# Performance work log

Hardware: AMD Instinct MI355X
Metric: run time of the kernel (lower is better)

The kernel has to match this reference:

```python
import jax, jax.numpy as jnp
import numpy as np

B, T, C = 2, 2048, 2048
NH, NKV = 16, 4
HD = C // NH  # 128


def setup_inputs() -> dict:
    key = jax.random.key(0)
    ks = jax.random.split(key, 5)
    w = lambda k, shape: jax.random.normal(k, shape, jnp.float32) * 0.02
    return {
        "x": jax.random.normal(ks[0], (B, T, C), jnp.float32),
        "Wq": w(ks[1], (C, C)),
        "Wk": w(ks[2], (C, NKV * HD)),
        "Wv": w(ks[3], (C, NKV * HD)),
        "Wproj": w(ks[4], (C, C)),
    }


def _rope(x):
    # x: [B, H, T, D]; rotate-half RoPE with base 10000
    D = x.shape[-1]
    t = x.shape[-2]
    inv_freq = 1.0 / (10000.0 ** (jnp.arange(0, D, 2, dtype=jnp.float32) / D))
    freqs = jnp.arange(t, dtype=jnp.float32)[:, None] * inv_freq[None, :]  # [T, D/2]
    emb = jnp.concatenate([freqs, freqs], axis=-1)  # [T, D]
    cos, sin = jnp.cos(emb), jnp.sin(emb)
    x1, x2 = x[..., : D // 2], x[..., D // 2 :]
    rotated = jnp.concatenate([-x2, x1], axis=-1)
    return x * cos + rotated * sin


def reference(x, Wq, Wk, Wv, Wproj):
    b, t, c = x.shape
    q = (x @ Wq).reshape(b, t, NH, HD).transpose(0, 2, 1, 3)    # [B,NH,T,HD]
    k = (x @ Wk).reshape(b, t, NKV, HD).transpose(0, 2, 1, 3)   # [B,NKV,T,HD]
    v = (x @ Wv).reshape(b, t, NKV, HD).transpose(0, 2, 1, 3)
    q = _rope(q)
    k = _rope(k)
    rep = NH // NKV
    k = jnp.repeat(k, rep, axis=1)  # [B,NH,T,HD]
    v = jnp.repeat(v, rep, axis=1)
    scale = 1.0 / jnp.sqrt(jnp.float32(HD))
    scores = jnp.einsum("bhqd,bhkd->bhqk", q, k) * scale        # [B,NH,T,T]
    causal = jnp.tril(jnp.ones((t, t), dtype=bool))
    scores = jnp.where(causal, scores, jnp.finfo(scores.dtype).min)
    attn = jax.nn.softmax(scores, axis=-1)
    y = jnp.einsum("bhqk,bhkd->bhqd", attn, v)                  # [B,NH,T,HD]
    y = y.transpose(0, 2, 1, 3).reshape(b, t, c)
    return y @ Wproj
```

## Files before the change

kernel.cpp:

```cpp
#include <hip/hip_runtime.h>

#define B_ 2
#define T_ 2048
#define C_ 2048
#define NH_ 16
#define NKV_ 4
#define HD_ 128
#define M_ 4096
#define NQKV_ 3072

typedef __bf16 bf16x8 __attribute__((ext_vector_type(8)));
typedef float f32x4 __attribute__((ext_vector_type(4)));
typedef float f32x16 __attribute__((ext_vector_type(16)));

__device__ __forceinline__ unsigned short f2bf(float f) {
  union { float f; unsigned u; } c{f};
  unsigned u = c.u + 0x7FFFu + ((c.u >> 16) & 1u);
  return (unsigned short)(u >> 16);
}
__device__ __forceinline__ float bf2f(unsigned short h) {
  union { unsigned u; float f; } c{(unsigned)h << 16};
  return c.f;
}

#define GLOAD_LDS16(g, l)                                        \
  __builtin_amdgcn_global_load_lds(                              \
      (const __attribute__((address_space(1))) void*)(g),        \
      (__attribute__((address_space(3))) void*)(l), 16, 0, 0)

__global__ void rope_table_kernel(float2* __restrict__ rt) {
  int t = blockIdx.x, i = threadIdx.x;
  float inv = powf(10000.f, -(float)(2 * i) / 128.f);
  float s, c;
  sincosf((float)t * inv, &s, &c);
  rt[t * 64 + i] = make_float2(c, s);
}

__global__ void convx_kernel(const float* __restrict__ x, unsigned short* __restrict__ xb, int n4) {
  int i = blockIdx.x * blockDim.x + threadIdx.x;
  if (i >= n4) return;
  float4 v = reinterpret_cast<const float4*>(x)[i];
  union { ushort4 u; unsigned short s[4]; } o;
  o.s[0] = f2bf(v.x); o.s[1] = f2bf(v.y); o.s[2] = f2bf(v.z); o.s[3] = f2bf(v.w);
  reinterpret_cast<ushort4*>(xb)[i] = o.u;
}

__global__ void transpose_conv_kernel(const float* __restrict__ W, unsigned short* __restrict__ Wt,
                                      int K, int N) {
  __shared__ float tile[32][33];
  int bx = blockIdx.x * 32;
  int by = blockIdx.y * 32;
  int tx = threadIdx.x & 31, ty = threadIdx.x >> 5;
#pragma unroll
  for (int r = 0; r < 32; r += 8)
    tile[ty + r][tx] = W[(size_t)(by + ty + r) * N + bx + tx];
  __syncthreads();
#pragma unroll
  for (int r = 0; r < 32; r += 8)
    Wt[(size_t)(bx + ty + r) * K + by + tx] = f2bf(tile[tx][ty + r]);
}

__global__ void rope_kernel(unsigned short* __restrict__ qkv, const float2* __restrict__ rt) {
  int g = blockIdx.x * blockDim.x + threadIdx.x;
  if (g >= M_ * 160) return;
  int m = g / 160, u = g - m * 160;
  int t = m & (T_ - 1);
  int io, col0;
  if (u < 128) { io = (u & 7) * 8; col0 = (u >> 3) * HD_ + io; }
  else         { int uu = u - 128; io = (uu & 7) * 8; col0 = C_ + (uu >> 3) * HD_ + io; }
  unsigned short* p = qkv + (size_t)m * NQKV_ + col0;
  union V8 { uint4 v; unsigned short s[8]; };
  V8 a, b, oa, ob;
  a.v = *reinterpret_cast<const uint4*>(p);
  b.v = *reinterpret_cast<const uint4*>(p + 64);
#pragma unroll
  for (int j = 0; j < 8; ++j) {
    float2 cs = rt[t * 64 + io + j];
    float x1 = bf2f(a.s[j]), x2 = bf2f(b.s[j]);
    oa.s[j] = f2bf(x1 * cs.x - x2 * cs.y);
    ob.s[j] = f2bf(x2 * cs.x + x1 * cs.y);
  }
  *reinterpret_cast<uint4*>(p) = oa.v;
  *reinterpret_cast<uint4*>(p + 64) = ob.v;
}

__global__ void transpose_v_kernel(const unsigned short* __restrict__ qkv,
                                   unsigned short* __restrict__ vt) {
  __shared__ unsigned short tile[32][33];
  int bh = blockIdx.z;
  int b = bh >> 2, kvh = bh & 3;
  int t0 = blockIdx.x * 32, d0 = blockIdx.y * 32;
  int tx = threadIdx.x & 31, ty = threadIdx.x >> 5;
#pragma unroll
  for (int r = 0; r < 32; r += 8)
    tile[ty + r][tx] = qkv[(size_t)(b * T_ + t0 + ty + r) * NQKV_ + 2560 + kvh * HD_ + d0 + tx];
  __syncthreads();
#pragma unroll
  for (int r = 0; r < 32; r += 8)
    vt[(size_t)(bh * HD_ + d0 + ty + r) * T_ + t0 + tx] = tile[tx][ty + r];
}

template <typename OUT>
__global__ __launch_bounds__(256) void gemm_bf16(const unsigned short* __restrict__ A,
                                                 const unsigned short* __restrict__ Bt,
                                                 OUT* __restrict__ Cm,
                                                 int M, int N, int K) {
  constexpr int BK = 32;
  __shared__ __align__(16) unsigned short Al[2][128 * BK];
  __shared__ __align__(16) unsigned short Bl[2][128 * BK];
  int tid = threadIdx.x, w = tid >> 6, lane = tid & 63;
  int l15 = lane & 15, l4 = lane >> 4;
  int wr = w >> 1, wc = w & 1;
  size_t arow0 = (size_t)blockIdx.y * 128;
  size_t brow0 = (size_t)blockIdx.x * 128;

  f32x4 acc[4][4];
#pragma unroll
  for (int mi = 0; mi < 4; ++mi)
#pragma unroll
    for (int ni = 0; ni < 4; ++ni) acc[mi][ni] = (f32x4){0.f, 0.f, 0.f, 0.f};

  auto stage = [&](int buf, int k0) {
#pragma unroll
    for (int i = 0; i < 2; ++i) {
      int c = i * 256 + w * 64 + lane;
      const unsigned short* g = A + (arow0 + (c >> 2)) * K + k0 + (c & 3) * 8;
      GLOAD_LDS16(g, &Al[buf][(i * 4 + w) * 512]);
    }
#pragma unroll
    for (int i = 0; i < 2; ++i) {
      int c = i * 256 + w * 64 + lane;
      const unsigned short* g = Bt + (brow0 + (c >> 2)) * K + k0 + (c & 3) * 8;
      GLOAD_LDS16(g, &Bl[buf][(i * 4 + w) * 512]);
    }
  };

  stage(0, 0);
  __syncthreads();
  int NT = K / BK, cur = 0;
  for (int kt = 0; kt < NT; ++kt) {
    if (kt + 1 < NT) stage(cur ^ 1, (kt + 1) * BK);
    const unsigned short* Ab = &Al[cur][0];
    const unsigned short* Bb = &Bl[cur][0];
    bf16x8 af[4], bfr[4];
#pragma unroll
    for (int mi = 0; mi < 4; ++mi)
      af[mi] = *reinterpret_cast<const bf16x8*>(Ab + (wr * 64 + mi * 16 + l15) * BK + l4 * 8);
#pragma unroll
    for (int ni = 0; ni < 4; ++ni)
      bfr[ni] = *reinterpret_cast<const bf16x8*>(Bb + (wc * 64 + ni * 16 + l15) * BK + l4 * 8);
#pragma unroll
    for (int mi = 0; mi < 4; ++mi)
#pragma unroll
      for (int ni = 0; ni < 4; ++ni)
        acc[mi][ni] = __builtin_amdgcn_mfma_f32_16x16x32_bf16(af[mi], bfr[ni], acc[mi][ni], 0, 0, 0);
    __syncthreads();
    cur ^= 1;
  }

#pragma unroll
  for (int mi = 0; mi < 4; ++mi)
#pragma unroll
    for (int ni = 0; ni < 4; ++ni) {
      size_t row = arow0 + wr * 64 + mi * 16 + l4 * 4;
      size_t col = brow0 + wc * 64 + ni * 16 + l15;
#pragma unroll
      for (int r = 0; r < 4; ++r) {
        float v = acc[mi][ni][r];
        if constexpr (sizeof(OUT) == 4) Cm[(row + r) * N + col] = v;
        else                            Cm[(row + r) * N + col] = f2bf(v);
      }
    }
}

__global__ __launch_bounds__(256, 2) void attn_kernel(const unsigned short* __restrict__ qkv,
                                                      const unsigned short* __restrict__ vt,
                                                      unsigned short* __restrict__ att) {
  constexpr int KB = 64;
  __shared__ __align__(16) unsigned short Kl[2][KB * 128];
  __shared__ __align__(16) unsigned short Vl[2][128 * KB];
  int tid = threadIdx.x, w = tid >> 6, lane = tid & 63;
  int l31 = lane & 31, hi = lane >> 5;
  int h4 = hi * 4;

  int id = blockIdx.x;
  int u = id & 255, half = id >> 8;
  int bh = u & 31;
  int qh = u >> 5;
  int qi = half ? (15 - qh) : qh;
  int q0 = qi * 128;
  int b = bh >> 4, hd = bh & 15, kvh = hd >> 2;
  int qr0 = q0 + w * 32;
  int ql = qr0 + l31;

  bf16x8 qf[8];
  {
    const unsigned short* qb = qkv + (size_t)(b * T_ + ql) * NQKV_ + hd * HD_ + hi * 8;
    const float scale = 0.08838834764831845f;
#pragma unroll
    for (int df = 0; df < 8; ++df) {
      bf16x8 t = *reinterpret_cast<const bf16x8*>(qb + df * 16);
#pragma unroll
      for (int j = 0; j < 8; ++j) t[j] = (__bf16)((float)t[j] * scale);
      qf[df] = t;
    }
  }

  f32x16 o[4];
#pragma unroll
  for (int dt = 0; dt < 4; ++dt)
#pragma unroll
    for (int r = 0; r < 16; ++r) o[dt][r] = 0.f;
  float mr = -1e30f, lr = 0.f;

  auto stage = [&](int buf, int kv0) {
#pragma unroll
    for (int i = 0; i < 4; ++i) {
      int c = (i * 4 + w) * 64 + lane;
      int g = c ^ ((c >> 4) & 7);
      const unsigned short* src =
          qkv + (size_t)(b * T_ + kv0 + (g >> 4)) * NQKV_ + C_ + kvh * HD_ + (g & 15) * 8;
      GLOAD_LDS16(src, &Kl[buf][(i * 4 + w) * 512]);
    }
#pragma unroll
    for (int i = 0; i < 4; ++i) {
      int c = (i * 4 + w) * 64 + lane;
      int g = c ^ ((c >> 3) & 7);
      const unsigned short* src =
          vt + (size_t)((b * NKV_ + kvh) * HD_ + (g >> 3)) * T_ + kv0 + (g & 7) * 8;
      GLOAD_LDS16(src, &Vl[buf][(i * 4 + w) * 512]);
    }
  };

  int nt = q0 / KB + 2;
  stage(0, 0);
  __syncthreads();
  int cur = 0;
  for (int kt = 0; kt < nt; ++kt) {
    int kv0 = kt * KB;
    if (kt + 1 < nt) stage(cur ^ 1, kv0 + KB);

    if (kv0 <= qr0 + 31) {
      f32x16 s[2];
#pragma unroll
      for (int r = 0; r < 16; ++r) { s[0][r] = 0.f; s[1][r] = 0.f; }
      __builtin_amdgcn_s_setprio(1);
#pragma unroll
      for (int t2 = 0; t2 < 2; ++t2)
#pragma unroll
        for (int df = 0; df < 8; ++df) {
          bf16x8 kf = *reinterpret_cast<const bf16x8*>(
              &Kl[cur][((t2 * 32 + l31) * 128 + df * 16 + hi * 8) ^ ((l31 & 7) << 3)]);
          s[t2] = __builtin_amdgcn_mfma_f32_32x32x16_bf16(kf, qf[df], s[t2], 0, 0, 0);
        }
      __builtin_amdgcn_s_setprio(0);

      bool need_mask = (kv0 + KB - 1) > qr0;
      float rm = -1e30f;
#pragma unroll
      for (int t2 = 0; t2 < 2; ++t2)
#pragma unroll
        for (int r = 0; r < 16; ++r) {
          float sv = s[t2][r];
          int kcol = kv0 + t2 * 32 + (r & 3) + 8 * (r >> 2) + h4;
          if (need_mask && kcol > ql) sv = -1e30f;
          s[t2][r] = sv;
          rm = fmaxf(rm, sv);
        }
      rm = fmaxf(rm, __shfl_xor(rm, 32));

      if (!__all(rm <= mr + 8.f)) {
        float mnew = fmaxf(mr, rm);
        float alpha = __expf(mr - mnew);
        mr = mnew;
        lr *= alpha;
#pragma unroll
        for (int dt = 0; dt < 4; ++dt)
#pragma unroll
          for (int r = 0; r < 16; ++r) o[dt][r] *= alpha;
      }

      float ps = 0.f;
#pragma unroll
      for (int t2 = 0; t2 < 2; ++t2)
#pragma unroll
        for (int r = 0; r < 16; ++r) {
          float p = __expf(s[t2][r] - mr);
          s[t2][r] = p;
          ps += p;
        }
      lr += ps;

      unsigned pk[2][8];
#pragma unroll
      for (int t2 = 0; t2 < 2; ++t2)
#pragma unroll
        for (int i = 0; i < 8; ++i) {
          union { unsigned u32; __bf16 hh[2]; } pr;
          pr.hh[0] = (__bf16)s[t2][2 * i];
          pr.hh[1] = (__bf16)s[t2][2 * i + 1];
          pk[t2][i] = pr.u32;
        }

      bf16x8 pb[4];
#pragma unroll
      for (int f = 0; f < 4; ++f) {
        int t2 = f >> 1, bq = (f & 1) * 4;
        union { bf16x8 v; unsigned d[4]; } fr;
#pragma unroll
        for (int p = 0; p < 2; ++p) {
          unsigned uu = pk[t2][bq + p];
          unsigned ww = pk[t2][bq + 2 + p];
          unsigned us = (unsigned)__shfl_xor((int)uu, 32);
          unsigned ws = (unsigned)__shfl_xor((int)ww, 32);
          fr.d[p]     = hi ? ws : uu;
          fr.d[2 + p] = hi ? ww : us;
        }
        pb[f] = fr.v;
      }

      __builtin_amdgcn_s_setprio(1);
#pragma unroll
      for (int dt = 0; dt < 4; ++dt)
#pragma unroll
        for (int kf = 0; kf < 4; ++kf) {
          bf16x8 vf = *reinterpret_cast<const bf16x8*>(
              &Vl[cur][((dt * 32 + l31) * KB + kf * 16 + hi * 8) ^ ((l31 & 7) << 3)]);
          o[dt] = __builtin_amdgcn_mfma_f32_32x32x16_bf16(vf, pb[kf], o[dt], 0, 0, 0);
        }
      __builtin_amdgcn_s_setprio(0);
    }

    __syncthreads();
    cur ^= 1;
  }

  float ls = lr + __shfl_xor(lr, 32);
  float inv = 1.f / ls;
  unsigned short* ob = att + (size_t)(b * T_ + ql) * C_ + hd * HD_;
#pragma unroll
  for (int dt = 0; dt < 4; ++dt)
#pragma unroll
    for (int r = 0; r < 16; ++r) {
      int d = dt * 32 + (r & 3) + 8 * (r >> 2) + h4;
      ob[d] = f2bf(o[dt][r] * inv);
    }
}

extern "C" void kernel_launch(void* const* d_in, const int* in_sizes, int n_in,
                              void* d_out, int out_size, void* d_ws, size_t ws_size,
                              hipStream_t stream) {
  const float* x  = (const float*)d_in[0];
  const float* Wq = (const float*)d_in[1];
  const float* Wk = (const float*)d_in[2];
  const float* Wv = (const float*)d_in[3];
  const float* Wp = (const float*)d_in[4];
  float* out = (float*)d_out;
  char* ws = (char*)d_ws;

  unsigned short* xb  = (unsigned short*)(ws);
  unsigned short* wt  = (unsigned short*)(ws + 16777216);
  unsigned short* qkv = (unsigned short*)(ws + 37748736);
  float2*         rt  = (float2*)(ws + 62914560);
  unsigned short* vt  = (unsigned short*)(ws + 63963136);
  unsigned short* att = xb;

  rope_table_kernel<<<T_, 64, 0, stream>>>(rt);
  convx_kernel<<<(M_ * C_ / 4 + 255) / 256, 256, 0, stream>>>(x, xb, M_ * C_ / 4);
  transpose_conv_kernel<<<dim3(64, 64), 256, 0, stream>>>(Wq, wt, C_, C_);
  transpose_conv_kernel<<<dim3(16, 64), 256, 0, stream>>>(Wk, wt + (size_t)2048 * 2048, C_, 512);
  transpose_conv_kernel<<<dim3(16, 64), 256, 0, stream>>>(Wv, wt + (size_t)2560 * 2048, C_, 512);
  transpose_conv_kernel<<<dim3(64, 64), 256, 0, stream>>>(Wp, wt + (size_t)3072 * 2048, C_, 2048);

  gemm_bf16<unsigned short><<<dim3(NQKV_ / 128, M_ / 128), 256, 0, stream>>>(
      xb, wt, qkv, M_, NQKV_, C_);
  rope_kernel<<<(M_ * 160 + 255) / 256, 256, 0, stream>>>(qkv, rt);
  transpose_v_kernel<<<dim3(T_ / 32, HD_ / 32, B_ * NKV_), 256, 0, stream>>>(qkv, vt);
  attn_kernel<<<dim3(512), 256, 0, stream>>>(qkv, vt, att);
  gemm_bf16<float><<<dim3(C_ / 128, M_ / 128), 256, 0, stream>>>(
      att, wt + (size_t)3072 * 2048, out, M_, C_, C_);
}
```

Baseline: 234.0 us.

## Fuse RoPE into QKV GEMM epilogue, merge weight transposes, use exp2 softmax

```diff
diff --git a/kernel.cpp b/kernel.cpp
--- a/kernel.cpp
+++ b/kernel.cpp
@@ -45,11 +45,20 @@
   reinterpret_cast<ushort4*>(xb)[i] = o.u;
 }
 
-__global__ void transpose_conv_kernel(const float* __restrict__ W, unsigned short* __restrict__ Wt,
-                                      int K, int N) {
+__global__ void transpose_conv4_kernel(const float* __restrict__ Wq, const float* __restrict__ Wk,
+                                       const float* __restrict__ Wv, const float* __restrict__ Wp,
+                                       unsigned short* __restrict__ wt) {
   __shared__ float tile[32][33];
-  int bx = blockIdx.x * 32;
-  int by = blockIdx.y * 32;
+  int id = blockIdx.x;
+  const float* W;
+  unsigned short* Wt;
+  int N, bx, by;
+  if (id < 4096)      { W = Wq; Wt = wt;                          N = 2048; int u = id;        bx = u & 63; by = u >> 6; }
+  else if (id < 5120) { W = Wk; Wt = wt + (size_t)2048 * 2048;    N = 512;  int u = id - 4096; bx = u & 15; by = u >> 4; }
+  else if (id < 6144) { W = Wv; Wt = wt + (size_t)2560 * 2048;    N = 512;  int u = id - 5120; bx = u & 15; by = u >> 4; }
+  else                { W = Wp; Wt = wt + (size_t)3072 * 2048;    N = 2048; int u = id - 6144; bx = u & 63; by = u >> 6; }
+  const int K = 2048;
+  bx *= 32; by *= 32;
   int tx = threadIdx.x & 31, ty = threadIdx.x >> 5;
 #pragma unroll
   for (int r = 0; r < 32; r += 8)
@@ -58,30 +67,6 @@
 #pragma unroll
   for (int r = 0; r < 32; r += 8)
     Wt[(size_t)(bx + ty + r) * K + by + tx] = f2bf(tile[tx][ty + r]);
-}
-
-__global__ void rope_kernel(unsigned short* __restrict__ qkv, const float2* __restrict__ rt) {
-  int g = blockIdx.x * blockDim.x + threadIdx.x;
-  if (g >= M_ * 160) return;
-  int m = g / 160, u = g - m * 160;
-  int t = m & (T_ - 1);
-  int io, col0;
-  if (u < 128) { io = (u & 7) * 8; col0 = (u >> 3) * HD_ + io; }
-  else         { int uu = u - 128; io = (uu & 7) * 8; col0 = C_ + (uu >> 3) * HD_ + io; }
-  unsigned short* p = qkv + (size_t)m * NQKV_ + col0;
-  union V8 { uint4 v; unsigned short s[8]; };
-  V8 a, b, oa, ob;
-  a.v = *reinterpret_cast<const uint4*>(p);
-  b.v = *reinterpret_cast<const uint4*>(p + 64);
-#pragma unroll
-  for (int j = 0; j < 8; ++j) {
-    float2 cs = rt[t * 64 + io + j];
-    float x1 = bf2f(a.s[j]), x2 = bf2f(b.s[j]);
-    oa.s[j] = f2bf(x1 * cs.x - x2 * cs.y);
-    ob.s[j] = f2bf(x2 * cs.x + x1 * cs.y);
-  }
-  *reinterpret_cast<uint4*>(p) = oa.v;
-  *reinterpret_cast<uint4*>(p + 64) = ob.v;
 }
 
 __global__ void transpose_v_kernel(const unsigned short* __restrict__ qkv,
@@ -100,25 +85,25 @@
     vt[(size_t)(bh * HD_ + d0 + ty + r) * T_ + t0 + tx] = tile[tx][ty + r];
 }
 
-template <typename OUT>
+template <typename OUT, bool ROPE>
 __global__ __launch_bounds__(256) void gemm_bf16(const unsigned short* __restrict__ A,
                                                  const unsigned short* __restrict__ Bt,
                                                  OUT* __restrict__ Cm,
+                                                 const float2* __restrict__ rt,
                                                  int M, int N, int K) {
   constexpr int BK = 32;
   __shared__ __align__(16) unsigned short Al[2][128 * BK];
   __shared__ __align__(16) unsigned short Bl[2][128 * BK];
   int tid = threadIdx.x, w = tid >> 6, lane = tid & 63;
   int l15 = lane & 15, l4 = lane >> 4;
-  int wr = w >> 1, wc = w & 1;
   size_t arow0 = (size_t)blockIdx.y * 128;
   size_t brow0 = (size_t)blockIdx.x * 128;
 
-  f32x4 acc[4][4];
-#pragma unroll
-  for (int mi = 0; mi < 4; ++mi)
-#pragma unroll
-    for (int ni = 0; ni < 4; ++ni) acc[mi][ni] = (f32x4){0.f, 0.f, 0.f, 0.f};
+  f32x4 acc[2][8];
+#pragma unroll
+  for (int mi = 0; mi < 2; ++mi)
+#pragma unroll
+    for (int ni = 0; ni < 8; ++ni) acc[mi][ni] = (f32x4){0.f, 0.f, 0.f, 0.f};
 
   auto stage = [&](int buf, int k0) {
 #pragma unroll
@@ -142,33 +127,46 @@
     if (kt + 1 < NT) stage(cur ^ 1, (kt + 1) * BK);
     const unsigned short* Ab = &Al[cur][0];
     const unsigned short* Bb = &Bl[cur][0];
-    bf16x8 af[4], bfr[4];
-#pragma unroll
-    for (int mi = 0; mi < 4; ++mi)
-      af[mi] = *reinterpret_cast<const bf16x8*>(Ab + (wr * 64 + mi * 16 + l15) * BK + l4 * 8);
-#pragma unroll
-    for (int ni = 0; ni < 4; ++ni)
-      bfr[ni] = *reinterpret_cast<const bf16x8*>(Bb + (wc * 64 + ni * 16 + l15) * BK + l4 * 8);
-#pragma unroll
-    for (int mi = 0; mi < 4; ++mi)
-#pragma unroll
-      for (int ni = 0; ni < 4; ++ni)
+    bf16x8 af[2], bfr[8];
+#pragma unroll
+    for (int mi = 0; mi < 2; ++mi)
+      af[mi] = *reinterpret_cast<const bf16x8*>(Ab + (w * 32 + mi * 16 + l15) * BK + l4 * 8);
+#pragma unroll
+    for (int ni = 0; ni < 8; ++ni)
+      bfr[ni] = *reinterpret_cast<const bf16x8*>(Bb + (ni * 16 + l15) * BK + l4 * 8);
+#pragma unroll
+    for (int mi = 0; mi < 2; ++mi)
+#pragma unroll
+      for (int ni = 0; ni < 8; ++ni)
         acc[mi][ni] = __builtin_amdgcn_mfma_f32_16x16x32_bf16(af[mi], bfr[ni], acc[mi][ni], 0, 0, 0);
     __syncthreads();
     cur ^= 1;
   }
 
-#pragma unroll
-  for (int mi = 0; mi < 4; ++mi)
-#pragma unroll
-    for (int ni = 0; ni < 4; ++ni) {
-      size_t row = arow0 + wr * 64 + mi * 16 + l4 * 4;
-      size_t col = brow0 + wc * 64 + ni * 16 + l15;
-#pragma unroll
-      for (int r = 0; r < 4; ++r) {
-        float v = acc[mi][ni][r];
-        if constexpr (sizeof(OUT) == 4) Cm[(row + r) * N + col] = v;
-        else                            Cm[(row + r) * N + col] = f2bf(v);
+  bool dorope = ROPE && (brow0 < 2560);
+#pragma unroll
+  for (int mi = 0; mi < 2; ++mi)
+#pragma unroll
+    for (int r = 0; r < 4; ++r) {
+      size_t row = arow0 + w * 32 + mi * 16 + l4 * 4 + r;
+      if (dorope) {
+        int t = (int)(row & (T_ - 1));
+#pragma unroll
+        for (int ni = 0; ni < 4; ++ni) {
+          float2 cs = rt[t * 64 + ni * 16 + l15];
+          float a1 = acc[mi][ni][r], a2 = acc[mi][ni + 4][r];
+          size_t col = brow0 + ni * 16 + l15;
+          Cm[row * N + col]      = f2bf(a1 * cs.x - a2 * cs.y);
+          Cm[row * N + col + 64] = f2bf(a2 * cs.x + a1 * cs.y);
+        }
+      } else {
+#pragma unroll
+        for (int ni = 0; ni < 8; ++ni) {
+          size_t col = brow0 + ni * 16 + l15;
+          float v = acc[mi][ni][r];
+          if constexpr (sizeof(OUT) == 4) Cm[row * N + col] = v;
+          else                            Cm[row * N + col] = f2bf(v);
+        }
       }
     }
 }
@@ -196,7 +194,7 @@
   bf16x8 qf[8];
   {
     const unsigned short* qb = qkv + (size_t)(b * T_ + ql) * NQKV_ + hd * HD_ + hi * 8;
-    const float scale = 0.08838834764831845f;
+    const float scale = 0.08838834764831845f * 1.4426950408889634f;
 #pragma unroll
     for (int df = 0; df < 8; ++df) {
       bf16x8 t = *reinterpret_cast<const bf16x8*>(qb + df * 16);
@@ -244,34 +242,41 @@
       f32x16 s[2];
 #pragma unroll
       for (int r = 0; r < 16; ++r) { s[0][r] = 0.f; s[1][r] = 0.f; }
+      const unsigned short* Kb = &Kl[cur][0];
       __builtin_amdgcn_s_setprio(1);
 #pragma unroll
       for (int t2 = 0; t2 < 2; ++t2)
 #pragma unroll
         for (int df = 0; df < 8; ++df) {
           bf16x8 kf = *reinterpret_cast<const bf16x8*>(
-              &Kl[cur][((t2 * 32 + l31) * 128 + df * 16 + hi * 8) ^ ((l31 & 7) << 3)]);
+              Kb + (((t2 * 32 + l31) * 128 + df * 16 + hi * 8) ^ ((l31 & 7) << 3)));
           s[t2] = __builtin_amdgcn_mfma_f32_32x32x16_bf16(kf, qf[df], s[t2], 0, 0, 0);
         }
       __builtin_amdgcn_s_setprio(0);
 
-      bool need_mask = (kv0 + KB - 1) > qr0;
       float rm = -1e30f;
-#pragma unroll
-      for (int t2 = 0; t2 < 2; ++t2)
-#pragma unroll
-        for (int r = 0; r < 16; ++r) {
-          float sv = s[t2][r];
-          int kcol = kv0 + t2 * 32 + (r & 3) + 8 * (r >> 2) + h4;
-          if (need_mask && kcol > ql) sv = -1e30f;
-          s[t2][r] = sv;
-          rm = fmaxf(rm, sv);
-        }
+      if ((kv0 + KB - 1) > qr0) {
+#pragma unroll
+        for (int t2 = 0; t2 < 2; ++t2)
+#pragma unroll
+          for (int r = 0; r < 16; ++r) {
+            float sv = s[t2][r];
+            int kcol = kv0 + t2 * 32 + (r & 3) + 8 * (r >> 2) + h4;
+            if (kcol > ql) sv = -1e30f;
+            s[t2][r] = sv;
+            rm = fmaxf(rm, sv);
+          }
+      } else {
+#pragma unroll
+        for (int t2 = 0; t2 < 2; ++t2)
+#pragma unroll
+          for (int r = 0; r < 16; ++r) rm = fmaxf(rm, s[t2][r]);
+      }
       rm = fmaxf(rm, __shfl_xor(rm, 32));
 
-      if (!__all(rm <= mr + 8.f)) {
+      if (!__all(rm <= mr + 11.0f)) {
         float mnew = fmaxf(mr, rm);
-        float alpha = __expf(mr - mnew);
+        float alpha = exp2f(mr - mnew);
         mr = mnew;
         lr *= alpha;
 #pragma unroll
@@ -285,7 +290,7 @@
       for (int t2 = 0; t2 < 2; ++t2)
 #pragma unroll
         for (int r = 0; r < 16; ++r) {
-          float p = __expf(s[t2][r] - mr);
+          float p = exp2f(s[t2][r] - mr);
           s[t2][r] = p;
           ps += p;
         }
@@ -319,13 +324,14 @@
         pb[f] = fr.v;
       }
 
+      const unsigned short* Vb = &Vl[cur][0];
       __builtin_amdgcn_s_setprio(1);
 #pragma unroll
       for (int dt = 0; dt < 4; ++dt)
 #pragma unroll
         for (int kf = 0; kf < 4; ++kf) {
           bf16x8 vf = *reinterpret_cast<const bf16x8*>(
-              &Vl[cur][((dt * 32 + l31) * KB + kf * 16 + hi * 8) ^ ((l31 & 7) << 3)]);
+              Vb + (((dt * 32 + l31) * KB + kf * 16 + hi * 8) ^ ((l31 & 7) << 3)));
           o[dt] = __builtin_amdgcn_mfma_f32_32x32x16_bf16(vf, pb[kf], o[dt], 0, 0, 0);
         }
       __builtin_amdgcn_s_setprio(0);
@@ -367,16 +373,12 @@
 
   rope_table_kernel<<<T_, 64, 0, stream>>>(rt);
   convx_kernel<<<(M_ * C_ / 4 + 255) / 256, 256, 0, stream>>>(x, xb, M_ * C_ / 4);
-  transpose_conv_kernel<<<dim3(64, 64), 256, 0, stream>>>(Wq, wt, C_, C_);
-  transpose_conv_kernel<<<dim3(16, 64), 256, 0, stream>>>(Wk, wt + (size_t)2048 * 2048, C_, 512);
-  transpose_conv_kernel<<<dim3(16, 64), 256, 0, stream>>>(Wv, wt + (size_t)2560 * 2048, C_, 512);
-  transpose_conv_kernel<<<dim3(64, 64), 256, 0, stream>>>(Wp, wt + (size_t)3072 * 2048, C_, 2048);
-
-  gemm_bf16<unsigned short><<<dim3(NQKV_ / 128, M_ / 128), 256, 0, stream>>>(
-      xb, wt, qkv, M_, NQKV_, C_);
-  rope_kernel<<<(M_ * 160 + 255) / 256, 256, 0, stream>>>(qkv, rt);
+  transpose_conv4_kernel<<<dim3(10240), 256, 0, stream>>>(Wq, Wk, Wv, Wp, wt);
+
+  gemm_bf16<unsigned short, true><<<dim3(NQKV_ / 128, M_ / 128), 256, 0, stream>>>(
+      xb, wt, qkv, rt, M_, NQKV_, C_);
   transpose_v_kernel<<<dim3(T_ / 32, HD_ / 32, B_ * NKV_), 256, 0, stream>>>(qkv, vt);
   attn_kernel<<<dim3(512), 256, 0, stream>>>(qkv, vt, att);
-  gemm_bf16<float><<<dim3(C_ / 128, M_ / 128), 256, 0, stream>>>(
-      att, wt + (size_t)3072 * 2048, out, M_, C_, C_);
-}
+  gemm_bf16<float, false><<<dim3(C_ / 128, M_ / 128), 256, 0, stream>>>(
+      att, wt + (size_t)3072 * 2048, out, nullptr, M_, C_, C_);
+}
```

Measured after the change: 220.2 us. -5.9%, faster.
